# Performance work log

Hardware: AMD Instinct MI355X
Metric: run time of the kernel (lower is better)

Reference implementation:

```python
import jax, jax.numpy as jnp
import numpy as np

GROUPS = 32
EPS = 1e-6


def _group_norm(x, scale, bias):
    B, C, H, W = x.shape
    xg = x.reshape(B, GROUPS, C // GROUPS, H, W)
    mean = xg.mean(axis=(2, 3, 4), keepdims=True)
    var = xg.var(axis=(2, 3, 4), keepdims=True)
    xg = (xg - mean) * jax.lax.rsqrt(var + EPS)
    x = xg.reshape(B, C, H, W)
    return x * scale[None, :, None, None] + bias[None, :, None, None]


def setup_inputs() -> dict:
    key = jax.random.key(0)
    ks = jax.random.split(key, 8)
    B, C, H, W = 4, 256, 64, 64
    s = 1.0 / np.sqrt(C)
    return {
        "x": jax.random.normal(ks[0], (B, C, H, W), jnp.float32),
        "gn_scale": jnp.ones((C,), jnp.float32),
        "gn_bias": jnp.zeros((C,), jnp.float32),
        "wq": jax.random.normal(ks[1], (C, C), jnp.float32) * s,
        "bq": jnp.zeros((C,), jnp.float32),
        "wk": jax.random.normal(ks[2], (C, C), jnp.float32) * s,
        "bk": jnp.zeros((C,), jnp.float32),
        "wv": jax.random.normal(ks[3], (C, C), jnp.float32) * s,
        "bv": jnp.zeros((C,), jnp.float32),
        "wp": jax.random.normal(ks[4], (C, C), jnp.float32) * s,
        "bp": jnp.zeros((C,), jnp.float32),
    }


def reference(x, gn_scale, gn_bias, wq, bq, wk, bk, wv, bv, wp, bp):
    B, C, H, W = x.shape
    hw = H * W
    o = _group_norm(x, gn_scale, gn_bias)           # [B,C,H,W]
    of = o.reshape(B, C, hw)                         # [B,C,hw]
    # 1x1 convs == per-pixel channel matmuls
    q = jnp.einsum('oc,bcn->bno', wq, of) + bq[None, None, :]   # [B,hw,C]
    k = jnp.einsum('oc,bcn->bon', wk, of) + bk[None, :, None]   # [B,C,hw]
    v = jnp.einsum('oc,bcn->bon', wv, of) + bv[None, :, None]   # [B,C,hw]
    w = jnp.einsum('bic,bcj->bij', q, k) * (C ** -0.5)          # [B,hw,hw]
    w = jax.nn.softmax(w, axis=2)
    # o[b,c,i] = sum_j v[b,c,j] * w[b,i,j]
    attn = jnp.einsum('bcj,bij->bci', v, w)          # [B,C,hw]
    # faithful to original: reshape to (B,C,W,H) (requires H==W)
    attn = attn.reshape(B, C, W, H)
    out = jnp.einsum('oc,bchw->bohw', wp, attn) + bp[None, :, None, None]
    return out + x
```

## Files before the change

### kernel.cpp

```cpp
#include <hip/hip_runtime.h>
#include <hip/hip_bf16.h>

#define NB 4
#define NC 256
#define NHW 4096
#define CPG 8
#define GEPS 1e-6f

typedef __hip_bfloat16 bf16;
typedef __attribute__((ext_vector_type(8))) short bf16x8;
typedef __attribute__((ext_vector_type(4))) float f32x4;
typedef __attribute__((ext_vector_type(8))) unsigned short u16x8;

#define MFMA16(A,B,C) __builtin_amdgcn_mfma_f32_16x16x32_bf16(A,B,C,0,0,0)

typedef __attribute__((address_space(1))) const unsigned int as1_uint;
typedef __attribute__((address_space(3))) unsigned int as3_uint;
__device__ __forceinline__ void gload_lds16(const void* g, void* l){
  __builtin_amdgcn_global_load_lds((as1_uint*)g, (as3_uint*)l, 16, 0, 0);
}

__device__ __forceinline__ float u2f(unsigned short u){
  union { unsigned u32; float f; } w; w.u32 = ((unsigned)u) << 16; return w.f;
}
__device__ __forceinline__ bf16 f2b(float v){ return __float2bfloat16(v); }
__device__ __forceinline__ unsigned short f2bu(float v){
  union { bf16 h; unsigned short u; } w; w.h = __float2bfloat16(v); return w.u;
}

__global__ __launch_bounds__(256)
void gn_stats_kernel(const float* __restrict__ x, float* __restrict__ stats){
  const int bg = blockIdx.x;
  const float* p = x + (size_t)bg * (CPG * NHW);
  float s = 0.f, s2 = 0.f;
  for(int i = threadIdx.x * 4; i < CPG * NHW; i += 1024){
    float4 v = *(const float4*)(p + i);
    s  += v.x + v.y + v.z + v.w;
    s2 += v.x*v.x + v.y*v.y + v.z*v.z + v.w*v.w;
  }
  __shared__ float red[256];
  red[threadIdx.x] = s; __syncthreads();
  for(int t = 128; t > 0; t >>= 1){
    if(threadIdx.x < t) red[threadIdx.x] += red[threadIdx.x + t];
    __syncthreads();
  }
  float sum = red[0]; __syncthreads();
  red[threadIdx.x] = s2; __syncthreads();
  for(int t = 128; t > 0; t >>= 1){
    if(threadIdx.x < t) red[threadIdx.x] += red[threadIdx.x + t];
    __syncthreads();
  }
  if(threadIdx.x == 0){
    const float inv_n = 1.f / (float)(CPG * NHW);
    float mean = sum * inv_n;
    float var = red[0] * inv_n - mean * mean;
    if(var < 0.f) var = 0.f;
    stats[bg * 2]     = mean;
    stats[bg * 2 + 1] = rsqrtf(var + GEPS);
  }
}

__global__ __launch_bounds__(256)
void wprep_kernel(const float* __restrict__ wq, const float* __restrict__ wk,
                  const float* __restrict__ wv, const float* __restrict__ wp,
                  const float* __restrict__ bq, const float* __restrict__ bk,
                  const float* __restrict__ bv,
                  bf16* __restrict__ wqkv, bf16* __restrict__ wpb, float* __restrict__ bqs){
  int i = blockIdx.x * 256 + threadIdx.x;
  if(i < 196608){
    float v;
    if(i < 65536)       v = wq[i] * 0.0625f;
    else if(i < 131072) v = wk[i - 65536];
    else                v = wv[i - 131072];
    wqkv[i] = f2b(v);
  } else {
    int j = i - 196608;
    wpb[j] = f2b(wp[j]);
  }
  if(i < 768) bqs[i] = (i < 256) ? bq[i] * 0.0625f : (i < 512 ? bk[i - 256] : bv[i - 512]);
}

__global__ __launch_bounds__(256)
void gn_prep_kernel(const float* __restrict__ x, const float* __restrict__ stats,
                    const float* __restrict__ gsc, const float* __restrict__ gbi,
                    bf16* __restrict__ xt){
  const int b = blockIdx.z, cB = blockIdx.y * 64, nB = blockIdx.x * 64;
  __shared__ unsigned short Tt[64][80];
  const int tid = threadIdx.x;
  const float* xb = x + ((size_t)(b * NC + cB)) * NHW + nB;
  #pragma unroll
  for(int pass = 0; pass < 4; pass++){
    int c_loc = (tid >> 4) + pass * 16;
    int n0 = (tid & 15) * 4;
    float4 v = *(const float4*)(xb + (size_t)c_loc * NHW + n0);
    int c_abs = cB + c_loc, bg = b * 32 + (c_abs >> 3);
    float a = stats[bg * 2 + 1] * gsc[c_abs];
    float d = gbi[c_abs] - stats[bg * 2] * a;
    Tt[n0 + 0][c_loc] = f2bu(v.x * a + d);
    Tt[n0 + 1][c_loc] = f2bu(v.y * a + d);
    Tt[n0 + 2][c_loc] = f2bu(v.z * a + d);
    Tt[n0 + 3][c_loc] = f2bu(v.w * a + d);
  }
  __syncthreads();
  int n_loc = tid >> 2, cq = (tid & 3) * 16;
  u16x8 w0 = *(const u16x8*)&Tt[n_loc][cq];
  u16x8 w1 = *(const u16x8*)&Tt[n_loc][cq + 8];
  unsigned short* dst = (unsigned short*)xt + ((size_t)(b * NHW + nB + n_loc)) * NC + cB + cq;
  *(u16x8*)dst = w0;
  *(u16x8*)(dst + 8) = w1;
}

__global__ __launch_bounds__(256, 2)
void gemm_kernel(const bf16* __restrict__ Wb, const bf16* __restrict__ Bm,
                 const float* __restrict__ bias,
                 bf16* __restrict__ qo, bf16* __restrict__ ko, bf16* __restrict__ vo,
                 float* __restrict__ fo, const float* __restrict__ xres, int epi){
  const int nB = blockIdx.x * 128;
  const int oB = blockIdx.y * 128;
  const int tid = threadIdx.x;
  const int wave = tid >> 6, lane = tid & 63;
  const int l15 = lane & 15, quad = lane >> 4;
  const int wx = wave & 1, wy = wave >> 1;

  __shared__ __align__(16) unsigned short Ast[2][512 * 8];
  __shared__ __align__(16) unsigned short Bst[2][512 * 8];
  __shared__ __align__(16) unsigned short Tt[128 * 136];

  const short* Wp = (const short*)Wb;
  const short* Bp = (const short*)Bm;

  f32x4 acc[4][4];
  #pragma unroll
  for(int mi = 0; mi < 4; mi++)
    #pragma unroll
    for(int ni = 0; ni < 4; ni++) acc[mi][ni] = (f32x4){0.f, 0.f, 0.f, 0.f};

  #pragma unroll
  for(int t = 0; t < 2; t++){
    int qn0 = (wave * 2 + t) * 64, qn = qn0 + lane;
    int o = qn >> 2, slot = qn & 3;
    gload_lds16(Wp + (size_t)(oB + o) * NC + ((slot ^ (o & 3)) * 8), &Ast[0][qn0 * 8]);
  }
  #pragma unroll
  for(int t = 0; t < 2; t++){
    int qn0 = (wave * 2 + t) * 64, qn = qn0 + lane;
    int n = qn >> 2, slot = qn & 3;
    gload_lds16(Bp + (size_t)(nB + n) * NC + ((slot ^ (n & 3)) * 8), &Bst[0][qn0 * 8]);
  }

  for(int kt = 0; kt < 8; kt++){
    __syncthreads();
    const int p = kt & 1;
    if(kt < 7){
      const int k0 = (kt + 1) * 32;
      #pragma unroll
      for(int t = 0; t < 2; t++){
        int qn0 = (wave * 2 + t) * 64, qn = qn0 + lane;
        int o = qn >> 2, slot = qn & 3;
        gload_lds16(Wp + (size_t)(oB + o) * NC + k0 + ((slot ^ (o & 3)) * 8), &Ast[p ^ 1][qn0 * 8]);
      }
      #pragma unroll
      for(int t = 0; t < 2; t++){
        int qn0 = (wave * 2 + t) * 64, qn = qn0 + lane;
        int n = qn >> 2, slot = qn & 3;
        gload_lds16(Bp + (size_t)(nB + n) * NC + k0 + ((slot ^ (n & 3)) * 8), &Bst[p ^ 1][qn0 * 8]);
      }
    }
    bf16x8 Af[4], Bf[4];
    #pragma unroll
    for(int mi = 0; mi < 4; mi++){
      int o = wx * 64 + mi * 16 + l15;
      Af[mi] = *(const bf16x8*)&Ast[p][(o * 4 + (quad ^ (o & 3))) * 8];
    }
    #pragma unroll
    for(int ni = 0; ni < 4; ni++){
      int n = wy * 64 + ni * 16 + l15;
      Bf[ni] = *(const bf16x8*)&Bst[p][(n * 4 + (quad ^ (n & 3))) * 8];
    }
    #pragma unroll
    for(int mi = 0; mi < 4; mi++)
      #pragma unroll
      for(int ni = 0; ni < 4; ni++)
        acc[mi][ni] = MFMA16(Af[mi], Bf[ni], acc[mi][ni]);
  }

  float bi[4][4];
  #pragma unroll
  for(int mi = 0; mi < 4; mi++)
    #pragma unroll
    for(int r = 0; r < 4; r++)
      bi[mi][r] = bias[oB + wx * 64 + mi * 16 + quad * 4 + r];

  if(epi == 1){
    #pragma unroll
    for(int mi = 0; mi < 4; mi++){
      #pragma unroll
      for(int ni = 0; ni < 4; ni++){
        int na = nB + wy * 64 + ni * 16 + l15;
        #pragma unroll
        for(int r = 0; r < 4; r++){
          int c = oB + wx * 64 + mi * 16 + quad * 4 + r;
          size_t idx = ((size_t)(na >> 12) * NC + c) * NHW + (na & 4095);
          fo[idx] = acc[mi][ni][r] + bi[mi][r] + xres[idx];
        }
      }
    }
  } else if(oB >= 512){
    #pragma unroll
    for(int mi = 0; mi < 4; mi++){
      #pragma unroll
      for(int ni = 0; ni < 4; ni++){
        int na = nB + wy * 64 + ni * 16 + l15;
        #pragma unroll
        for(int r = 0; r < 4; r++){
          int c = oB - 512 + wx * 64 + mi * 16 + quad * 4 + r;
          vo[((size_t)(na >> 12) * NC + c) * NHW + (na & 4095)] = f2b(acc[mi][ni][r] + bi[mi][r]);
        }
      }
    }
  } else {
    #pragma unroll
    for(int mi = 0; mi < 4; mi++){
      int ob = wx * 64 + mi * 16 + quad * 4;
      #pragma unroll
      for(int ni = 0; ni < 4; ni++){
        int nl = wy * 64 + ni * 16 + l15;
        ushort4 pk;
        pk.x = f2bu(acc[mi][ni][0] + bi[mi][0]);
        pk.y = f2bu(acc[mi][ni][1] + bi[mi][1]);
        pk.z = f2bu(acc[mi][ni][2] + bi[mi][2]);
        pk.w = f2bu(acc[mi][ni][3] + bi[mi][3]);
        *(ushort4*)&Tt[nl * 136 + ob] = pk;
      }
    }
    __syncthreads();
    bf16* dst = (oB < 256) ? qo : ko;
    const int oc0 = oB & 255;
    int row = tid >> 1, half = tid & 1;
    unsigned short* gp = (unsigned short*)dst + (size_t)(nB + row) * NC + oc0 + half * 64;
    #pragma unroll
    for(int j = 0; j < 8; j++){
      u16x8 w = *(const u16x8*)&Tt[row * 136 + half * 64 + j * 8];
      *(u16x8*)(gp + j * 8) = w;
    }
  }
}

__global__ __launch_bounds__(256, 2)
void flash_mfma4_kernel(const bf16* __restrict__ qg, const bf16* __restrict__ ktg,
                        const bf16* __restrict__ vg, bf16* __restrict__ Opart,
                        float* __restrict__ lpart){
  const int b = blockIdx.y, h = blockIdx.z;
  const int i0 = blockIdx.x * 128;
  const int tid = threadIdx.x;
  const int wave = tid >> 6, lane = tid & 63;
  const int l15 = lane & 15, quad = lane >> 4;

  __shared__ __align__(16) unsigned short Kt[2][1024 * 8];
  __shared__ __align__(16) unsigned short Vt[2][1024 * 8];
  __shared__ __align__(16) unsigned short Pt_all[4][32 * 40];
  unsigned short* Pt = Pt_all[wave];

  bf16x8 Qf[2][8];
  #pragma unroll
  for(int ist = 0; ist < 2; ist++){
    const short* qp = (const short*)qg +
        ((size_t)b * NHW + i0 + wave * 32 + ist * 16 + l15) * NC + quad * 8;
    #pragma unroll
    for(int ks = 0; ks < 8; ks++) Qf[ist][ks] = *(const bf16x8*)(qp + ks * 32);
  }

  const short* kb = (const short*)ktg + ((size_t)b * NHW + h * 1024) * NC;
  const short* vb = (const short*)vg + (size_t)b * NC * NHW + h * 1024;

  f32x4 O[2][16];
  #pragma unroll
  for(int ist = 0; ist < 2; ist++)
    #pragma unroll
    for(int ct = 0; ct < 16; ct++) O[ist][ct] = (f32x4){0.f, 0.f, 0.f, 0.f};
  float lr0 = 0.f, lr1 = 0.f;

  #pragma unroll
  for(int t = 0; t < 4; t++){
    int qn0 = (wave * 4 + t) * 64, qn = qn0 + lane;
    int j = qn >> 5, slot = qn & 31;
    gload_lds16(kb + (size_t)j * NC + ((slot ^ (j & 7)) * 8), &Kt[0][qn0 * 8]);
  }
  #pragma unroll
  for(int t = 0; t < 4; t++){
    int qn0 = (wave * 4 + t) * 64, qn = qn0 + lane;
    int c = qn >> 2, slot = qn & 3;
    gload_lds16(vb + (size_t)c * NHW + ((slot ^ (c & 3)) * 8), &Vt[0][qn0 * 8]);
  }

  for(int jt = 0; jt < 32; jt++){
    __syncthreads();
    const int p = jt & 1;
    if(jt < 31){
      const int j0n = (jt + 1) * 32;
      #pragma unroll
      for(int t = 0; t < 4; t++){
        int qn0 = (wave * 4 + t) * 64, qn = qn0 + lane;
        int j = qn >> 5, slot = qn & 31;
        gload_lds16(kb + (size_t)(j0n + j) * NC + ((slot ^ (j & 7)) * 8), &Kt[p ^ 1][qn0 * 8]);
      }
      #pragma unroll
      for(int t = 0; t < 4; t++){
        int qn0 = (wave * 4 + t) * 64, qn = qn0 + lane;
        int c = qn >> 2, slot = qn & 3;
        gload_lds16(vb + (size_t)c * NHW + j0n + ((slot ^ (c & 3)) * 8), &Vt[p ^ 1][qn0 * 8]);
      }
    }
    f32x4 S[2][2];
    #pragma unroll
    for(int st = 0; st < 2; st++){
      S[st][0] = (f32x4){0.f, 0.f, 0.f, 0.f};
      S[st][1] = (f32x4){0.f, 0.f, 0.f, 0.f};
      const int j = st * 16 + l15;
      const unsigned short* kr = &Kt[p][(size_t)j * 256];
      #pragma unroll
      for(int ks = 0; ks < 8; ks++){
        int slot = (ks * 4 + quad) ^ (j & 7);
        bf16x8 kf = *(const bf16x8*)&kr[slot * 8];
        S[st][0] = MFMA16(kf, Qf[0][ks], S[st][0]);
        S[st][1] = MFMA16(kf, Qf[1][ks], S[st][1]);
      }
    }
    #pragma unroll
    for(int ist = 0; ist < 2; ist++){
      #pragma unroll
      for(int st = 0; st < 2; st++){
        f32x4 sv = S[st][ist];
        float p0 = __expf(sv[0]), p1 = __expf(sv[1]);
        float p2 = __expf(sv[2]), p3 = __expf(sv[3]);
        if(ist == 0) lr0 += (p0 + p1) + (p2 + p3);
        else         lr1 += (p0 + p1) + (p2 + p3);
        ushort4 pk; pk.x = f2bu(p0); pk.y = f2bu(p1); pk.z = f2bu(p2); pk.w = f2bu(p3);
        *(ushort4*)&Pt[(ist * 16 + l15) * 40 + st * 16 + quad * 4] = pk;
      }
    }
    bf16x8 Pf0 = *(const bf16x8*)&Pt[(l15) * 40 + quad * 8];
    bf16x8 Pf1 = *(const bf16x8*)&Pt[(16 + l15) * 40 + quad * 8];
    #pragma unroll
    for(int ct = 0; ct < 16; ct++){
      int c = ct * 16 + l15;
      bf16x8 vf = *(const bf16x8*)&Vt[p][(c * 4 + (quad ^ (c & 3))) * 8];
      O[0][ct] = MFMA16(Pf0, vf, O[0][ct]);
      O[1][ct] = MFMA16(Pf1, vf, O[1][ct]);
    }
  }

  lr0 += __shfl_xor(lr0, 16); lr0 += __shfl_xor(lr0, 32);
  lr1 += __shfl_xor(lr1, 16); lr1 += __shfl_xor(lr1, 32);

  const size_t hb = (size_t)(h * NB + b) * NHW;
  #pragma unroll
  for(int ist = 0; ist < 2; ist++){
    #pragma unroll
    for(int r = 0; r < 4; r++){
      int i = i0 + wave * 32 + ist * 16 + quad * 4 + r;
      unsigned short* od = (unsigned short*)Opart + (hb + i) * NC + l15;
      #pragma unroll
      for(int ct = 0; ct < 16; ct++) od[ct * 16] = f2bu(O[ist][ct][r]);
    }
  }
  if(lane < 16){
    lpart[hb + i0 + wave * 32 + l15]      = lr0;
    lpart[hb + i0 + wave * 32 + 16 + l15] = lr1;
  }
}

__global__ __launch_bounds__(256)
void flash_combine4_kernel(const bf16* __restrict__ Opart, const float* __restrict__ lpart,
                           bf16* __restrict__ attn){
  int t = blockIdx.x * 256 + threadIdx.x;
  int ng = t >> 3;
  int c0 = (t & 7) * 32;
  const int HS = NB * NHW;
  float l = lpart[ng] + lpart[HS + ng] + lpart[2 * HS + ng] + lpart[3 * HS + ng];
  float inv = 1.f / l;
  const unsigned short* O0 = (const unsigned short*)Opart + (size_t)ng * NC + c0;
  unsigned short* dst = (unsigned short*)attn + (size_t)ng * NC + c0;
  #pragma unroll
  for(int u = 0; u < 32; u += 8){
    u16x8 a0 = *(const u16x8*)(O0 + u);
    u16x8 a1 = *(const u16x8*)(O0 + (size_t)HS * NC + u);
    u16x8 a2 = *(const u16x8*)(O0 + (size_t)2 * HS * NC + u);
    u16x8 a3 = *(const u16x8*)(O0 + (size_t)3 * HS * NC + u);
    u16x8 o;
    #pragma unroll
    for(int e = 0; e < 8; e++)
      o[e] = f2bu((u2f(a0[e]) + u2f(a1[e]) + u2f(a2[e]) + u2f(a3[e])) * inv);
    *(u16x8*)(dst + u) = o;
  }
}

extern "C" void kernel_launch(void* const* d_in, const int* in_sizes, int n_in,
                              void* d_out, int out_size, void* d_ws, size_t ws_size,
                              hipStream_t stream){
  (void)in_sizes; (void)n_in; (void)out_size; (void)ws_size;
  const float* x        = (const float*)d_in[0];
  const float* gn_scale = (const float*)d_in[1];
  const float* gn_bias  = (const float*)d_in[2];
  const float* wq = (const float*)d_in[3];  const float* bq = (const float*)d_in[4];
  const float* wk = (const float*)d_in[5];  const float* bk = (const float*)d_in[6];
  const float* wv = (const float*)d_in[7];  const float* bv = (const float*)d_in[8];
  const float* wp = (const float*)d_in[9];  const float* bp = (const float*)d_in[10];
  float* out = (float*)d_out;

  char* ws = (char*)d_ws;
  const size_t MB = 1048576;
  float* stats = (float*)ws;
  float* bqs   = (float*)(ws + 4096);
  bf16* wqkv   = (bf16*)(ws + 8192);
  bf16* wpb    = (bf16*)(ws + 8192 + 393216);
  bf16* xt     = (bf16*)(ws + 1 * MB);
  bf16* Opart  = xt;
  bf16* q      = (bf16*)(ws + 33 * MB);
  bf16* k      = (bf16*)(ws + 41 * MB);
  bf16* v      = (bf16*)(ws + 49 * MB);
  float* lpart = (float*)(ws + 57 * MB);
  bf16* attn   = q;

  gn_stats_kernel<<<128, 256, 0, stream>>>(x, stats);
  wprep_kernel<<<1024, 256, 0, stream>>>(wq, wk, wv, wp, bq, bk, bv, wqkv, wpb, bqs);
  gn_prep_kernel<<<dim3(64, 4, NB), 256, 0, stream>>>(x, stats, gn_scale, gn_bias, xt);

  gemm_kernel<<<dim3(128, 6), 256, 0, stream>>>(
      wqkv, xt, bqs, q, k, v, nullptr, nullptr, 0);

  flash_mfma4_kernel<<<dim3(32, NB, 4), 256, 0, stream>>>(q, k, v, Opart, lpart);
  flash_combine4_kernel<<<512, 256, 0, stream>>>(Opart, lpart, attn);

  gemm_kernel<<<dim3(128, 2), 256, 0, stream>>>(
      wpb, attn, bp, nullptr, nullptr, nullptr, out, x, 1);
}
```

Before: 223.1 us.

## Merge GN stats with weight prep, retune LDS swizzle, add MFMA priority hints

Folds the weight/bias bf16 conversion kernel into the group-norm statistics kernel as extra blocks, saving one launch. Changes the LDS XOR swizzle for 4-slot rows from (row&3) to ((row>>1)&3) in the GEMM and the flash V tile, aiming to cut bank conflicts on the 16-byte fragment reads. Also wraps the MFMA loops in s_setprio raises so waves issuing matrix ops get scheduling priority. The swizzle change alters conflict patterns and could help or hurt.

```diff
diff --git a/kernel.cpp b/kernel.cpp
--- a/kernel.cpp
+++ b/kernel.cpp
@@ -29,7 +29,28 @@
 }
 
 __global__ __launch_bounds__(256)
-void gn_stats_kernel(const float* __restrict__ x, float* __restrict__ stats){
+void gn_stats_wprep_kernel(const float* __restrict__ x, float* __restrict__ stats,
+                           const float* __restrict__ wq, const float* __restrict__ wk,
+                           const float* __restrict__ wv, const float* __restrict__ wp,
+                           const float* __restrict__ bq, const float* __restrict__ bk,
+                           const float* __restrict__ bv,
+                           bf16* __restrict__ wqkv, bf16* __restrict__ wpb,
+                           float* __restrict__ bqs){
+  if(blockIdx.x >= 128){
+    int i = (blockIdx.x - 128) * 256 + threadIdx.x;
+    if(i < 196608){
+      float v;
+      if(i < 65536)       v = wq[i] * 0.0625f;
+      else if(i < 131072) v = wk[i - 65536];
+      else                v = wv[i - 131072];
+      wqkv[i] = f2b(v);
+    } else {
+      int j = i - 196608;
+      wpb[j] = f2b(wp[j]);
+    }
+    if(i < 768) bqs[i] = (i < 256) ? bq[i] * 0.0625f : (i < 512 ? bk[i - 256] : bv[i - 512]);
+    return;
+  }
   const int bg = blockIdx.x;
   const float* p = x + (size_t)bg * (CPG * NHW);
   float s = 0.f, s2 = 0.f;
@@ -58,26 +79,6 @@
     stats[bg * 2]     = mean;
     stats[bg * 2 + 1] = rsqrtf(var + GEPS);
   }
-}
-
-__global__ __launch_bounds__(256)
-void wprep_kernel(const float* __restrict__ wq, const float* __restrict__ wk,
-                  const float* __restrict__ wv, const float* __restrict__ wp,
-                  const float* __restrict__ bq, const float* __restrict__ bk,
-                  const float* __restrict__ bv,
-                  bf16* __restrict__ wqkv, bf16* __restrict__ wpb, float* __restrict__ bqs){
-  int i = blockIdx.x * 256 + threadIdx.x;
-  if(i < 196608){
-    float v;
-    if(i < 65536)       v = wq[i] * 0.0625f;
-    else if(i < 131072) v = wk[i - 65536];
-    else                v = wv[i - 131072];
-    wqkv[i] = f2b(v);
-  } else {
-    int j = i - 196608;
-    wpb[j] = f2b(wp[j]);
-  }
-  if(i < 768) bqs[i] = (i < 256) ? bq[i] * 0.0625f : (i < 512 ? bk[i - 256] : bv[i - 512]);
 }
 
 __global__ __launch_bounds__(256)
@@ -139,13 +140,13 @@
   for(int t = 0; t < 2; t++){
     int qn0 = (wave * 2 + t) * 64, qn = qn0 + lane;
     int o = qn >> 2, slot = qn & 3;
-    gload_lds16(Wp + (size_t)(oB + o) * NC + ((slot ^ (o & 3)) * 8), &Ast[0][qn0 * 8]);
+    gload_lds16(Wp + (size_t)(oB + o) * NC + ((slot ^ ((o >> 1) & 3)) * 8), &Ast[0][qn0 * 8]);
   }
   #pragma unroll
   for(int t = 0; t < 2; t++){
     int qn0 = (wave * 2 + t) * 64, qn = qn0 + lane;
     int n = qn >> 2, slot = qn & 3;
-    gload_lds16(Bp + (size_t)(nB + n) * NC + ((slot ^ (n & 3)) * 8), &Bst[0][qn0 * 8]);
+    gload_lds16(Bp + (size_t)(nB + n) * NC + ((slot ^ ((n >> 1) & 3)) * 8), &Bst[0][qn0 * 8]);
   }
 
   for(int kt = 0; kt < 8; kt++){
@@ -157,31 +158,33 @@
       for(int t = 0; t < 2; t++){
         int qn0 = (wave * 2 + t) * 64, qn = qn0 + lane;
         int o = qn >> 2, slot = qn & 3;
-        gload_lds16(Wp + (size_t)(oB + o) * NC + k0 + ((slot ^ (o & 3)) * 8), &Ast[p ^ 1][qn0 * 8]);
+        gload_lds16(Wp + (size_t)(oB + o) * NC + k0 + ((slot ^ ((o >> 1) & 3)) * 8), &Ast[p ^ 1][qn0 * 8]);
       }
       #pragma unroll
       for(int t = 0; t < 2; t++){
         int qn0 = (wave * 2 + t) * 64, qn = qn0 + lane;
         int n = qn >> 2, slot = qn & 3;
-        gload_lds16(Bp + (size_t)(nB + n) * NC + k0 + ((slot ^ (n & 3)) * 8), &Bst[p ^ 1][qn0 * 8]);
+        gload_lds16(Bp + (size_t)(nB + n) * NC + k0 + ((slot ^ ((n >> 1) & 3)) * 8), &Bst[p ^ 1][qn0 * 8]);
       }
     }
     bf16x8 Af[4], Bf[4];
     #pragma unroll
     for(int mi = 0; mi < 4; mi++){
       int o = wx * 64 + mi * 16 + l15;
-      Af[mi] = *(const bf16x8*)&Ast[p][(o * 4 + (quad ^ (o & 3))) * 8];
+      Af[mi] = *(const bf16x8*)&Ast[p][(o * 4 + (quad ^ ((o >> 1) & 3))) * 8];
     }
     #pragma unroll
     for(int ni = 0; ni < 4; ni++){
       int n = wy * 64 + ni * 16 + l15;
-      Bf[ni] = *(const bf16x8*)&Bst[p][(n * 4 + (quad ^ (n & 3))) * 8];
-    }
+      Bf[ni] = *(const bf16x8*)&Bst[p][(n * 4 + (quad ^ ((n >> 1) & 3))) * 8];
+    }
+    __builtin_amdgcn_s_setprio(1);
     #pragma unroll
     for(int mi = 0; mi < 4; mi++)
       #pragma unroll
       for(int ni = 0; ni < 4; ni++)
         acc[mi][ni] = MFMA16(Af[mi], Bf[ni], acc[mi][ni]);
+    __builtin_amdgcn_s_setprio(0);
   }
 
   float bi[4][4];
@@ -290,7 +293,7 @@
   for(int t = 0; t < 4; t++){
     int qn0 = (wave * 4 + t) * 64, qn = qn0 + lane;
     int c = qn >> 2, slot = qn & 3;
-    gload_lds16(vb + (size_t)c * NHW + ((slot ^ (c & 3)) * 8), &Vt[0][qn0 * 8]);
+    gload_lds16(vb + (size_t)c * NHW + ((slot ^ ((c >> 1) & 3)) * 8), &Vt[0][qn0 * 8]);
   }
 
   for(int jt = 0; jt < 32; jt++){
@@ -308,10 +311,11 @@
       for(int t = 0; t < 4; t++){
         int qn0 = (wave * 4 + t) * 64, qn = qn0 + lane;
         int c = qn >> 2, slot = qn & 3;
-        gload_lds16(vb + (size_t)c * NHW + j0n + ((slot ^ (c & 3)) * 8), &Vt[p ^ 1][qn0 * 8]);
+        gload_lds16(vb + (size_t)c * NHW + j0n + ((slot ^ ((c >> 1) & 3)) * 8), &Vt[p ^ 1][qn0 * 8]);
       }
     }
     f32x4 S[2][2];
+    __builtin_amdgcn_s_setprio(1);
     #pragma unroll
     for(int st = 0; st < 2; st++){
       S[st][0] = (f32x4){0.f, 0.f, 0.f, 0.f};
@@ -326,6 +330,7 @@
         S[st][1] = MFMA16(kf, Qf[1][ks], S[st][1]);
       }
     }
+    __builtin_amdgcn_s_setprio(0);
     #pragma unroll
     for(int ist = 0; ist < 2; ist++){
       #pragma unroll
@@ -341,13 +346,15 @@
     }
     bf16x8 Pf0 = *(const bf16x8*)&Pt[(l15) * 40 + quad * 8];
     bf16x8 Pf1 = *(const bf16x8*)&Pt[(16 + l15) * 40 + quad * 8];
+    __builtin_amdgcn_s_setprio(1);
     #pragma unroll
     for(int ct = 0; ct < 16; ct++){
       int c = ct * 16 + l15;
-      bf16x8 vf = *(const bf16x8*)&Vt[p][(c * 4 + (quad ^ (c & 3))) * 8];
+      bf16x8 vf = *(const bf16x8*)&Vt[p][(c * 4 + (quad ^ ((c >> 1) & 3))) * 8];
       O[0][ct] = MFMA16(Pf0, vf, O[0][ct]);
       O[1][ct] = MFMA16(Pf1, vf, O[1][ct]);
     }
+    __builtin_amdgcn_s_setprio(0);
   }
 
   lr0 += __shfl_xor(lr0, 16); lr0 += __shfl_xor(lr0, 32);
@@ -422,8 +429,8 @@
   float* lpart = (float*)(ws + 57 * MB);
   bf16* attn   = q;
 
-  gn_stats_kernel<<<128, 256, 0, stream>>>(x, stats);
-  wprep_kernel<<<1024, 256, 0, stream>>>(wq, wk, wv, wp, bq, bk, bv, wqkv, wpb, bqs);
+  gn_stats_wprep_kernel<<<1152, 256, 0, stream>>>(
+      x, stats, wq, wk, wv, wp, bq, bk, bv, wqkv, wpb, bqs);
   gn_prep_kernel<<<dim3(64, 4, NB), 256, 0, stream>>>(x, stats, gn_scale, gn_bias, xt);
 
   gemm_kernel<<<dim3(128, 6), 256, 0, stream>>>(
```

After: 213.3 us. 4.4% less time.
